# Performance work log

Hardware: AMD Instinct MI355X
Metric: run time of the kernel (lower is better)

## Reference

```python
import jax, jax.numpy as jnp
import numpy as np

V, E, H, K = 8000, 100, 64, 17  # vocab, embed, hidden, num_tags (fixed by source)
B, T = 256, 512


def setup_inputs() -> dict:
    key = jax.random.key(0)
    ks = jax.random.split(key, 16)
    g = lambda i, shape: (jax.random.normal(ks[i], shape, jnp.float32) * 0.1)
    data = jax.random.randint(ks[0], (B, T), 0, V).astype(jnp.int32)
    mask = jnp.ones((B, T), dtype=bool)
    return {
        "data": data,
        "mask": mask,
        "emb": g(1, (V, E)),
        # PyTorch LSTM layout: gates stacked [i, f, g, o] along dim 0
        "Wih_f": g(2, (4 * H, E)), "Whh_f": g(3, (4 * H, H)),
        "bih_f": g(4, (4 * H,)), "bhh_f": g(5, (4 * H,)),
        "Wih_b": g(6, (4 * H, E)), "Whh_b": g(7, (4 * H, H)),
        "bih_b": g(8, (4 * H,)), "bhh_b": g(9, (4 * H,)),
        "W_out": g(10, (K, 2 * H)), "b_out": g(11, (K,)),
        "trans": g(12, (K, K)),            # trans[i, j] = score of i -> j
        "start_trans": g(13, (K,)),
        "end_trans": g(14, (K,)),
    }


def _lstm_dir(x, Wih, Whh, bih, bhh, reverse):
    # x: [B, T, E] -> hidden states [B, T, H]
    Bx, Tx, _ = x.shape
    Hx = Whh.shape[1]
    xs = jnp.swapaxes(x, 0, 1)  # [T, B, E]

    def step(carry, xt):
        h, c = carry
        gates = xt @ Wih.T + h @ Whh.T + bih + bhh  # [B, 4H]
        i, f, g, o = jnp.split(gates, 4, axis=-1)
        c = jax.nn.sigmoid(f) * c + jax.nn.sigmoid(i) * jnp.tanh(g)
        h = jax.nn.sigmoid(o) * jnp.tanh(c)
        return (h, c), h

    init = (jnp.zeros((Bx, Hx), x.dtype), jnp.zeros((Bx, Hx), x.dtype))
    _, hs = jax.lax.scan(step, init, xs, reverse=reverse)
    return jnp.swapaxes(hs, 0, 1)  # [B, T, H]


def _emissions(data, emb, Wih_f, Whh_f, bih_f, bhh_f, Wih_b, Whh_b, bih_b, bhh_b, W_out, b_out):
    x = emb[data]                                         # [B, T, E]
    hf = _lstm_dir(x, Wih_f, Whh_f, bih_f, bhh_f, False)  # [B, T, H]
    hb = _lstm_dir(x, Wih_b, Whh_b, bih_b, bhh_b, True)   # [B, T, H]
    h = jnp.concatenate([hf, hb], axis=-1)                # [B, T, 2H]
    return h @ W_out.T + b_out                            # [B, T, K]


def _viterbi(emission, mask, trans, start_trans, end_trans):
    Bx, Tx, Kx = emission.shape
    score = start_trans[None, :] + emission[:, 0]         # [B, K]
    em = jnp.swapaxes(emission, 0, 1)[1:]                 # [T-1, B, K]
    mk = jnp.swapaxes(mask, 0, 1)[1:]                     # [T-1, B]
    ident = jnp.arange(Kx)

    def step(score, inp):
        emit_t, m_t = inp
        # cand[b, i, j] = score[b, i] + trans[i, j] + emit_t[b, j]
        cand = score[:, :, None] + trans[None] + emit_t[:, None, :]
        new = cand.max(axis=1)
        bp = cand.argmax(axis=1)
        score = jnp.where(m_t[:, None], new, score)
        bp = jnp.where(m_t[:, None], bp, ident[None, :])
        return score, bp

    score, bps = jax.lax.scan(step, score, (em, mk))       # bps: [T-1, B, K]
    final = score + end_trans[None, :]
    best_score = final.max(axis=1)                         # [B]
    last = final.argmax(axis=1)                            # [B]

    def back(tag, bp_t):
        prev = jnp.take_along_axis(bp_t, tag[:, None], axis=1)[:, 0]
        return prev, prev

    _, prevs = jax.lax.scan(back, last, bps, reverse=True)  # [T-1, B]
    paths = jnp.concatenate([prevs, last[None, :]], axis=0).T  # [B, T]
    return best_score, paths


def reference(data, mask, emb, Wih_f, Whh_f, bih_f, bhh_f, Wih_b, Whh_b, bih_b, bhh_b,
              W_out, b_out, trans, start_trans, end_trans):
    emission = _emissions(data, emb, Wih_f, Whh_f, bih_f, bhh_f,
                          Wih_b, Whh_b, bih_b, bhh_b, W_out, b_out)
    return _viterbi(emission, mask, trans, start_trans, end_trans)
```

## Files before the change

### kernel.cpp

```cpp
#include <hip/hip_runtime.h>
#include <hip/hip_bf16.h>

typedef unsigned int u32;
typedef unsigned char u8;

#define B_ 256
#define T_ 512
#define E_ 100
#define H_ 64
#define K_ 17
#define V_ 8000

#define WS_G     0
#define WS_H     16384000
#define WS_EMIT  83492864
#define WS_BP    92405760
#define WS_LAST  96600064

__global__ __launch_bounds__(256) void k1_build_G(
    const float* __restrict__ emb,
    const float* __restrict__ Wih_f,
    const float* __restrict__ bih_f,
    const float* __restrict__ bhh_f,
    const float* __restrict__ Wih_b,
    const float* __restrict__ bih_b,
    const float* __restrict__ bhh_b,
    float* __restrict__ G)
{
  __shared__ float xl[32 * E_];
  int v0 = blockIdx.x * 32;
  int dir = blockIdx.y;
  int tid = threadIdx.x;
  const float* Wih = dir ? Wih_b : Wih_f;
  const float* bih = dir ? bih_b : bih_f;
  const float* bhh = dir ? bhh_b : bhh_f;

  for (int i = tid; i < 32 * E_; i += 256) xl[i] = emb[v0 * E_ + i];

  int u = tid >> 2, g = tid & 3;
  int row = (g << 6) + u;
  float4 A4[25];
  {
    const float4* wp = reinterpret_cast<const float4*>(Wih + row * E_);
#pragma unroll
    for (int q = 0; q < 25; ++q) A4[q] = wp[q];
  }
  float bias = __fadd_rn(bih[row], bhh[row]);
  __syncthreads();

  float* Gd = G + (size_t)dir * V_ * 256;
  for (int vi = 0; vi < 32; ++vi) {
    const float* xp = &xl[vi * E_];
    float a0 = bias, a1 = 0.f, a2 = 0.f, a3 = 0.f;
#pragma unroll
    for (int q = 0; q < 25; ++q) {
      float4 w4 = A4[q];
      float4 x4 = *reinterpret_cast<const float4*>(&xp[4 * q]);
      a0 = fmaf(w4.x, x4.x, a0);
      a1 = fmaf(w4.y, x4.y, a1);
      a2 = fmaf(w4.z, x4.z, a2);
      a3 = fmaf(w4.w, x4.w, a3);
    }
    Gd[(v0 + vi) * 256 + tid] = (a0 + a1) + (a2 + a3);
  }
}

__global__ __launch_bounds__(256) void k2_lstm(
    const int* __restrict__ data,
    const float* __restrict__ G,
    const float* __restrict__ Whh_f,
    const float* __restrict__ Whh_b,
    float* __restrict__ hout)
{
  __shared__ __align__(16) float hls[2][64];
  int bid = blockIdx.x;
  int b = bid & 255;
  int dir = bid >> 8;
  int tid = threadIdx.x;
  int w = tid >> 6, l = tid & 63;
  int u = (w << 4) + (l >> 2);
  int g = l & 3;
  int row = (g << 6) + u;
  const float* Whh = dir ? Whh_b : Whh_f;

  float W[64];
  {
    const float4* wp = reinterpret_cast<const float4*>(Whh + row * 64);
#pragma unroll
    for (int q = 0; q < 16; ++q) {
      float4 v = wp[q];
      W[q * 4 + 0] = v.x;
      W[q * 4 + 1] = v.y;
      W[q * 4 + 2] = v.z;
      W[q * 4 + 3] = v.w;
    }
  }
  if (tid < 64) hls[0][tid] = 0.0f;
  float c = 0.0f;
  const int* tokp = data + b * T_;
  const float* Gd = G + (size_t)dir * V_ * 256;
  float* hob = hout + ((size_t)(dir * B_ + b)) * T_ * H_;

  int tt0 = dir ? (T_ - 1) : 0;
  int tt1 = dir ? (T_ - 2) : 1;
  float g0 = Gd[(size_t)tokp[tt0] * 256 + tid];
  float g1 = Gd[(size_t)tokp[tt1] * 256 + tid];
  __syncthreads();

  int cur = 0;
  for (int s = 0; s < T_; ++s) {
    int tt = dir ? (T_ - 1 - s) : s;
    float g2 = 0.0f;
    if (s < T_ - 2) {
      int ttn = dir ? (T_ - 3 - s) : (s + 2);
      g2 = Gd[(size_t)tokp[ttn] * 256 + tid];
    }
    const float* hb_ = hls[cur];
    float a0 = g0, a1 = 0.f, a2 = 0.f, a3 = 0.f;
#pragma unroll
    for (int k4 = 0; k4 < 16; ++k4) {
      float4 h4 = *reinterpret_cast<const float4*>(&hb_[k4 * 4]);
      a0 = fmaf(W[k4 * 4 + 0], h4.x, a0);
      a1 = fmaf(W[k4 * 4 + 1], h4.y, a1);
      a2 = fmaf(W[k4 * 4 + 2], h4.z, a2);
      a3 = fmaf(W[k4 * 4 + 3], h4.w, a3);
    }
    float acc = ((a0 + a1) + a2) + a3;
    float act;
    if (g == 2) act = tanhf(acc);
    else        act = 1.0f / (1.0f + expf(-acc));
    int base = l & ~3;
    float iv = __shfl(act, base + 0, 64);
    float fv = __shfl(act, base + 1, 64);
    float gv = __shfl(act, base + 2, 64);
    float ov = __shfl(act, base + 3, 64);
    c = __fadd_rn(__fmul_rn(fv, c), __fmul_rn(iv, gv));
    float hn = __fmul_rn(ov, tanhf(c));
    if (g == 0) {
      hls[cur ^ 1][u] = hn;
      hob[tt * H_ + u] = hn;
    }
    __syncthreads();
    cur ^= 1;
    g0 = g1; g1 = g2;
  }
}

__global__ __launch_bounds__(256) void k3_emit(
    const float* __restrict__ hbuf,
    const float* __restrict__ W_out,
    const float* __restrict__ b_out,
    float* __restrict__ emit)
{
  __shared__ float hl[64][132];
  __shared__ float Wl[17][132];
  int tid = threadIdx.x;
  int p0 = blockIdx.x * 64;
  const float* hf = hbuf;
  const float* hb = hbuf + (size_t)B_ * T_ * H_;
#pragma unroll
  for (int i = 0; i < 4; ++i) {
    int idx = tid + i * 256;
    int pos = idx >> 4, e4 = idx & 15;
    float4 v = reinterpret_cast<const float4*>(hf + (size_t)p0 * 64)[idx];
    *reinterpret_cast<float4*>(&hl[pos][e4 * 4]) = v;
    float4 v2 = reinterpret_cast<const float4*>(hb + (size_t)p0 * 64)[idx];
    *reinterpret_cast<float4*>(&hl[pos][64 + e4 * 4]) = v2;
  }
  for (int i = tid; i < 17 * 128; i += 256) {
    int k = i >> 7, e = i & 127;
    Wl[k][e] = W_out[i];
  }
  __syncthreads();

  int pos = tid >> 2, ks = tid & 3;
  float acc[5] = {0.f, 0.f, 0.f, 0.f, 0.f};
#pragma unroll
  for (int e4 = 0; e4 < 32; ++e4) {
    float4 x4 = *reinterpret_cast<const float4*>(&hl[pos][e4 * 4]);
#pragma unroll
    for (int kk = 0; kk < 5; ++kk) {
      int k = ks + kk * 4;
      if (k < K_) {
        float4 w4 = *reinterpret_cast<const float4*>(&Wl[k][e4 * 4]);
        acc[kk] = fmaf(x4.x, w4.x, acc[kk]);
        acc[kk] = fmaf(x4.y, w4.y, acc[kk]);
        acc[kk] = fmaf(x4.z, w4.z, acc[kk]);
        acc[kk] = fmaf(x4.w, w4.w, acc[kk]);
      }
    }
  }
#pragma unroll
  for (int kk = 0; kk < 5; ++kk) {
    int k = ks + kk * 4;
    if (k < K_)
      emit[(size_t)(p0 + pos) * K_ + k] = __fadd_rn(acc[kk], b_out[k]);
  }
}

__global__ __launch_bounds__(64) void k4_viterbi(
    const float* __restrict__ emit,
    const float* __restrict__ trans,
    const float* __restrict__ start_trans,
    const float* __restrict__ end_trans,
    u8* __restrict__ bp,
    int* __restrict__ last,
    float* __restrict__ out)
{
  int b = blockIdx.x;
  int l = threadIdx.x;
  int ic = l >> 5;
  int j = l & 31;
  int jc = (j < K_) ? j : 0;
  int i0 = ic ? 9 : 0;
  int cnt = ic ? 8 : 9;
  float tr[9];
#pragma unroll
  for (int r = 0; r < 9; ++r) {
    int i = i0 + r;
    tr[r] = (r < cnt) ? trans[i * K_ + jc] : -__builtin_inff();
  }
  const float* eb = emit + (size_t)b * T_ * K_;
  float endt = end_trans[jc];
  float s = __fadd_rn(start_trans[jc], eb[jc]);
  u8* bpb = bp + (size_t)b * T_ * 32;
  float epre = eb[K_ + jc];

  for (int t = 1; t < T_; ++t) {
    float ej = epre;
    if (t + 1 < T_) epre = eb[(size_t)(t + 1) * K_ + jc];
    float sv[9];
#pragma unroll
    for (int r = 0; r < 9; ++r) sv[r] = __shfl(s, (l & 32) + i0 + r, 64);
    float m = __fadd_rn(__fadd_rn(sv[0], tr[0]), ej);
    int idx = i0;
#pragma unroll
    for (int r = 1; r < 9; ++r) {
      float cand = __fadd_rn(__fadd_rn(sv[r], tr[r]), ej);
      if (cand > m) { m = cand; idx = i0 + r; }
    }
    float m2 = __shfl_xor(m, 32, 64);
    int idx2 = __shfl_xor(idx, 32, 64);
    bool take = (m2 > m) || ((m2 == m) && (idx2 < idx));
    if (take) { m = m2; idx = idx2; }
    s = m;
    if (ic == 0 && j < K_) bpb[(size_t)(t - 1) * 32 + j] = (u8)idx;
  }
  float fin = __fadd_rn(s, endt);
  float bm = __shfl(fin, (l & 32), 64);
  int bi = 0;
#pragma unroll
  for (int jj = 1; jj < K_; ++jj) {
    float v = __shfl(fin, (l & 32) + jj, 64);
    if (v > bm) { bm = v; bi = jj; }
  }
  if (l == 0) {
    out[b] = bm;
    last[b] = bi;
    out[256 + (size_t)b * T_ + (T_ - 1)] = (float)bi;
  }
}

__global__ __launch_bounds__(64) void k5_backtrace(
    const u8* __restrict__ bp,
    const int* __restrict__ last,
    float* __restrict__ out)
{
  int b = blockIdx.x * 64 + threadIdx.x;
  const uint4* bpp = reinterpret_cast<const uint4*>(bp + (size_t)b * T_ * 32);
  int tag = last[b];
  uint4 A = bpp[510 * 2];
  uint4 Bv = bpp[510 * 2 + 1];
  for (int t = 510; t >= 0; --t) {
    uint4 A2 = A, B2 = Bv;
    if (t > 0) { A2 = bpp[(t - 1) * 2]; B2 = bpp[(t - 1) * 2 + 1]; }
    u32 dw = (tag < 8) ? ((tag < 4) ? A.x : A.y) : ((tag < 12) ? A.z : A.w);
    dw = (tag < 16) ? dw : Bv.x;
    tag = (int)((dw >> ((tag & 3) * 8)) & 0xffu);
    out[256 + (size_t)b * T_ + t] = (float)tag;
    A = A2; Bv = B2;
  }
}

extern "C" void kernel_launch(void* const* d_in, const int* in_sizes, int n_in,
                              void* d_out, int out_size, void* d_ws, size_t ws_size,
                              hipStream_t stream) {
  const int*   data  = (const int*)d_in[0];
  const float* emb   = (const float*)d_in[2];
  const float* Wih_f = (const float*)d_in[3];
  const float* Whh_f = (const float*)d_in[4];
  const float* bih_f = (const float*)d_in[5];
  const float* bhh_f = (const float*)d_in[6];
  const float* Wih_b = (const float*)d_in[7];
  const float* Whh_b = (const float*)d_in[8];
  const float* bih_b = (const float*)d_in[9];
  const float* bhh_b = (const float*)d_in[10];
  const float* W_out = (const float*)d_in[11];
  const float* b_out = (const float*)d_in[12];
  const float* trans = (const float*)d_in[13];
  const float* start_trans = (const float*)d_in[14];
  const float* end_trans   = (const float*)d_in[15];

  char* ws = (char*)d_ws;
  float* G    = (float*)(ws + WS_G);
  float* hbuf = (float*)(ws + WS_H);
  float* emit = (float*)(ws + WS_EMIT);
  u8*    bp   = (u8*)(ws + WS_BP);
  int*   lastp = (int*)(ws + WS_LAST);
  float* out = (float*)d_out;

  k1_build_G<<<dim3(250, 2), 256, 0, stream>>>(emb, Wih_f, bih_f, bhh_f,
                                               Wih_b, bih_b, bhh_b, G);
  k2_lstm<<<512, 256, 0, stream>>>(data, G, Whh_f, Whh_b, hbuf);
  k3_emit<<<2048, 256, 0, stream>>>(hbuf, W_out, b_out, emit);
  k4_viterbi<<<256, 64, 0, stream>>>(emit, trans, start_trans, end_trans,
                                     bp, lastp, out);
  k5_backtrace<<<4, 64, 0, stream>>>(bp, lastp, out);
}
```

Before: 784.9 us.

## Split LSTM dot products across thread pairs, use fast exp/rcp, batch backtrace loads

After: 716.5 us. -8.7%, faster.

```diff
diff --git a/kernel.cpp b/kernel.cpp
--- a/kernel.cpp
+++ b/kernel.cpp
@@ -65,7 +65,7 @@
   }
 }
 
-__global__ __launch_bounds__(256) void k2_lstm(
+__global__ __launch_bounds__(512, 4) void k2_lstm(
     const int* __restrict__ data,
     const float* __restrict__ G,
     const float* __restrict__ Whh_f,
@@ -78,16 +78,20 @@
   int dir = bid >> 8;
   int tid = threadIdx.x;
   int w = tid >> 6, l = tid & 63;
-  int u = (w << 4) + (l >> 2);
-  int g = l & 3;
+  int ul = l >> 3;
+  int r = l & 7;
+  int g = r >> 1;
+  int half = r & 1;
+  int u = (w << 3) + ul;
   int row = (g << 6) + u;
+  int gidx = (u << 2) + g;
   const float* Whh = dir ? Whh_b : Whh_f;
 
-  float W[64];
+  float W[32];
   {
-    const float4* wp = reinterpret_cast<const float4*>(Whh + row * 64);
-#pragma unroll
-    for (int q = 0; q < 16; ++q) {
+    const float4* wp = reinterpret_cast<const float4*>(Whh + row * 64 + half * 32);
+#pragma unroll
+    for (int q = 0; q < 8; ++q) {
       float4 v = wp[q];
       W[q * 4 + 0] = v.x;
       W[q * 4 + 1] = v.y;
@@ -95,16 +99,19 @@
       W[q * 4 + 3] = v.w;
     }
   }
+  const float L2E = 1.4426950408889634f;
+  float zs = (g == 2) ? (-2.0f * L2E) : (-L2E);
+  float ma = (g == 2) ? 2.0f : 1.0f;
+  float aa = (g == 2) ? -1.0f : 0.0f;
+
   if (tid < 64) hls[0][tid] = 0.0f;
   float c = 0.0f;
   const int* tokp = data + b * T_;
   const float* Gd = G + (size_t)dir * V_ * 256;
   float* hob = hout + ((size_t)(dir * B_ + b)) * T_ * H_;
 
-  int tt0 = dir ? (T_ - 1) : 0;
-  int tt1 = dir ? (T_ - 2) : 1;
-  float g0 = Gd[(size_t)tokp[tt0] * 256 + tid];
-  float g1 = Gd[(size_t)tokp[tt1] * 256 + tid];
+  float g0 = Gd[(size_t)tokp[dir ? (T_ - 1) : 0] * 256 + gidx];
+  float g1 = Gd[(size_t)tokp[dir ? (T_ - 2) : 1] * 256 + gidx];
   __syncthreads();
 
   int cur = 0;
@@ -113,30 +120,35 @@
     float g2 = 0.0f;
     if (s < T_ - 2) {
       int ttn = dir ? (T_ - 3 - s) : (s + 2);
-      g2 = Gd[(size_t)tokp[ttn] * 256 + tid];
-    }
-    const float* hb_ = hls[cur];
-    float a0 = g0, a1 = 0.f, a2 = 0.f, a3 = 0.f;
-#pragma unroll
-    for (int k4 = 0; k4 < 16; ++k4) {
+      g2 = Gd[(size_t)tokp[ttn] * 256 + gidx];
+    }
+    const float* hb_ = hls[cur] + (half << 5);
+    float a0 = (half == 0) ? g0 : 0.0f;
+    float a1 = 0.f, a2 = 0.f, a3 = 0.f;
+#pragma unroll
+    for (int k4 = 0; k4 < 8; ++k4) {
       float4 h4 = *reinterpret_cast<const float4*>(&hb_[k4 * 4]);
       a0 = fmaf(W[k4 * 4 + 0], h4.x, a0);
       a1 = fmaf(W[k4 * 4 + 1], h4.y, a1);
       a2 = fmaf(W[k4 * 4 + 2], h4.z, a2);
       a3 = fmaf(W[k4 * 4 + 3], h4.w, a3);
     }
-    float acc = ((a0 + a1) + a2) + a3;
-    float act;
-    if (g == 2) act = tanhf(acc);
-    else        act = 1.0f / (1.0f + expf(-acc));
-    int base = l & ~3;
+    float part = (a0 + a1) + (a2 + a3);
+    float full = part + __shfl_xor(part, 1, 64);
+    float ex = __builtin_amdgcn_exp2f(full * zs);
+    float sg = __builtin_amdgcn_rcpf(1.0f + ex);
+    float act = fmaf(ma, sg, aa);
+    int base = l & 56;
     float iv = __shfl(act, base + 0, 64);
-    float fv = __shfl(act, base + 1, 64);
-    float gv = __shfl(act, base + 2, 64);
-    float ov = __shfl(act, base + 3, 64);
+    float fv = __shfl(act, base + 2, 64);
+    float gv = __shfl(act, base + 4, 64);
+    float ov = __shfl(act, base + 6, 64);
     c = __fadd_rn(__fmul_rn(fv, c), __fmul_rn(iv, gv));
-    float hn = __fmul_rn(ov, tanhf(c));
-    if (g == 0) {
+    float tc = fmaf(2.0f,
+                    __builtin_amdgcn_rcpf(1.0f + __builtin_amdgcn_exp2f(c * (-2.0f * L2E))),
+                    -1.0f);
+    float hn = __fmul_rn(ov, tc);
+    if (r == 0) {
       hls[cur ^ 1][u] = hn;
       hob[tt * H_ + u] = hn;
     }
@@ -198,6 +210,8 @@
   }
 }
 
+#define AMAX(vA, iA, vB, iB) { bool tk_ = (vB) > (vA); if (tk_) { vA = (vB); iA = (iB); } }
+
 __global__ __launch_bounds__(64) void k4_viterbi(
     const float* __restrict__ emit,
     const float* __restrict__ trans,
@@ -210,35 +224,41 @@
   int b = blockIdx.x;
   int l = threadIdx.x;
   int ic = l >> 5;
+  int hbase = l & 32;
   int j = l & 31;
   int jc = (j < K_) ? j : 0;
   int i0 = ic ? 9 : 0;
   int cnt = ic ? 8 : 9;
   float tr[9];
 #pragma unroll
-  for (int r = 0; r < 9; ++r) {
-    int i = i0 + r;
-    tr[r] = (r < cnt) ? trans[i * K_ + jc] : -__builtin_inff();
-  }
+  for (int q = 0; q < 9; ++q)
+    tr[q] = (q < cnt) ? trans[(i0 + q) * K_ + jc] : -__builtin_inff();
   const float* eb = emit + (size_t)b * T_ * K_;
   float endt = end_trans[jc];
   float s = __fadd_rn(start_trans[jc], eb[jc]);
   u8* bpb = bp + (size_t)b * T_ * 32;
-  float epre = eb[K_ + jc];
+  float e0 = eb[K_ + jc];
+  float e1 = eb[2 * K_ + jc];
 
   for (int t = 1; t < T_; ++t) {
-    float ej = epre;
-    if (t + 1 < T_) epre = eb[(size_t)(t + 1) * K_ + jc];
+    float ej = e0;
+    e0 = e1;
+    if (t + 2 < T_) e1 = eb[(size_t)(t + 2) * K_ + jc];
     float sv[9];
 #pragma unroll
-    for (int r = 0; r < 9; ++r) sv[r] = __shfl(s, (l & 32) + i0 + r, 64);
-    float m = __fadd_rn(__fadd_rn(sv[0], tr[0]), ej);
-    int idx = i0;
-#pragma unroll
-    for (int r = 1; r < 9; ++r) {
-      float cand = __fadd_rn(__fadd_rn(sv[r], tr[r]), ej);
-      if (cand > m) { m = cand; idx = i0 + r; }
-    }
+    for (int q = 0; q < 9; ++q) sv[q] = __shfl(s, hbase + i0 + q, 64);
+    float cd[9];
+#pragma unroll
+    for (int q = 0; q < 9; ++q) cd[q] = __fadd_rn(__fadd_rn(sv[q], tr[q]), ej);
+    float v01 = cd[0]; int x01 = i0;     AMAX(v01, x01, cd[1], i0 + 1);
+    float v23 = cd[2]; int x23 = i0 + 2; AMAX(v23, x23, cd[3], i0 + 3);
+    float v45 = cd[4]; int x45 = i0 + 4; AMAX(v45, x45, cd[5], i0 + 5);
+    float v67 = cd[6]; int x67 = i0 + 6; AMAX(v67, x67, cd[7], i0 + 7);
+    AMAX(v01, x01, v23, x23);
+    AMAX(v45, x45, v67, x67);
+    AMAX(v01, x01, v45, x45);
+    AMAX(v01, x01, cd[8], i0 + 8);
+    float m = v01; int idx = x01;
     float m2 = __shfl_xor(m, 32, 64);
     int idx2 = __shfl_xor(idx, 32, 64);
     bool take = (m2 > m) || ((m2 == m) && (idx2 < idx));
@@ -247,11 +267,11 @@
     if (ic == 0 && j < K_) bpb[(size_t)(t - 1) * 32 + j] = (u8)idx;
   }
   float fin = __fadd_rn(s, endt);
-  float bm = __shfl(fin, (l & 32), 64);
+  float bm = __shfl(fin, hbase, 64);
   int bi = 0;
 #pragma unroll
   for (int jj = 1; jj < K_; ++jj) {
-    float v = __shfl(fin, (l & 32) + jj, 64);
+    float v = __shfl(fin, hbase + jj, 64);
     if (v > bm) { bm = v; bi = jj; }
   }
   if (l == 0) {
@@ -267,18 +287,60 @@
     float* __restrict__ out)
 {
   int b = blockIdx.x * 64 + threadIdx.x;
-  const uint4* bpp = reinterpret_cast<const uint4*>(bp + (size_t)b * T_ * 32);
+  const u8* base = bp + (size_t)b * T_ * 32;
   int tag = last[b];
-  uint4 A = bpp[510 * 2];
-  uint4 Bv = bpp[510 * 2 + 1];
-  for (int t = 510; t >= 0; --t) {
-    uint4 A2 = A, B2 = Bv;
-    if (t > 0) { A2 = bpp[(t - 1) * 2]; B2 = bpp[(t - 1) * 2 + 1]; }
-    u32 dw = (tag < 8) ? ((tag < 4) ? A.x : A.y) : ((tag < 12) ? A.z : A.w);
-    dw = (tag < 16) ? dw : Bv.x;
-    tag = (int)((dw >> ((tag & 3) * 8)) & 0xffu);
-    out[256 + (size_t)b * T_ + t] = (float)tag;
-    A = A2; Bv = B2;
+  float* ob = out + 256 + (size_t)b * T_;
+  uint4 A0[8], A1[8];
+  u32 B0[8], B1[8];
+#pragma unroll
+  for (int q = 0; q < 8; ++q) {
+    const u8* p = base + (size_t)(510 - q) * 32;
+    A0[q] = *reinterpret_cast<const uint4*>(p);
+    B0[q] = *reinterpret_cast<const u32*>(p + 16);
+  }
+  int t0 = 510;
+  for (int pair = 0; pair < 32; ++pair) {
+#pragma unroll
+    for (int q = 0; q < 8; ++q) {
+      int tn = t0 - 8 - q;
+      if (tn >= 0) {
+        const u8* p = base + (size_t)tn * 32;
+        A1[q] = *reinterpret_cast<const uint4*>(p);
+        B1[q] = *reinterpret_cast<const u32*>(p + 16);
+      }
+    }
+#pragma unroll
+    for (int q = 0; q < 8; ++q) {
+      int t = t0 - q;
+      if (t >= 0) {
+        uint4 Av = A0[q]; u32 Bw = B0[q];
+        u32 dw = (tag < 8) ? ((tag < 4) ? Av.x : Av.y) : ((tag < 12) ? Av.z : Av.w);
+        dw = (tag < 16) ? dw : Bw;
+        tag = (int)((dw >> ((tag & 3) * 8)) & 0xffu);
+        ob[t] = (float)tag;
+      }
+    }
+#pragma unroll
+    for (int q = 0; q < 8; ++q) {
+      int tn = t0 - 16 - q;
+      if (tn >= 0) {
+        const u8* p = base + (size_t)tn * 32;
+        A0[q] = *reinterpret_cast<const uint4*>(p);
+        B0[q] = *reinterpret_cast<const u32*>(p + 16);
+      }
+    }
+#pragma unroll
+    for (int q = 0; q < 8; ++q) {
+      int t = t0 - 8 - q;
+      if (t >= 0) {
+        uint4 Av = A1[q]; u32 Bw = B1[q];
+        u32 dw = (tag < 8) ? ((tag < 4) ? Av.x : Av.y) : ((tag < 12) ? Av.z : Av.w);
+        dw = (tag < 16) ? dw : Bw;
+        tag = (int)((dw >> ((tag & 3) * 8)) & 0xffu);
+        ob[t] = (float)tag;
+      }
+    }
+    t0 -= 16;
   }
 }
 
@@ -311,7 +373,7 @@
 
   k1_build_G<<<dim3(250, 2), 256, 0, stream>>>(emb, Wih_f, bih_f, bhh_f,
                                                Wih_b, bih_b, bhh_b, G);
-  k2_lstm<<<512, 256, 0, stream>>>(data, G, Whh_f, Whh_b, hbuf);
+  k2_lstm<<<512, 512, 0, stream>>>(data, G, Whh_f, Whh_b, hbuf);
   k3_emit<<<2048, 256, 0, stream>>>(hbuf, W_out, b_out, emit);
   k4_viterbi<<<256, 64, 0, stream>>>(emit, trans, start_trans, end_trans,
                                      bp, lastp, out);
```
